# Kernel optimization log

Measured on AMD Instinct MI355X. Metric: run time of the kernel, lower is better.

The kernel has to match this reference:

```python
import jax, jax.numpy as jnp
import numpy as np

EMB = 768
HEADS = 8

def setup_inputs() -> dict:
    key = jax.random.key(0)
    ks = jax.random.split(key, 9)
    B, N, E = 16, 1024, EMB
    s = 1.0 / np.sqrt(E)
    x = jax.random.normal(ks[0], (B, N, E), dtype=jnp.float32)
    Wq = jax.random.normal(ks[1], (E, E), dtype=jnp.float32) * s
    bq = jnp.zeros((E,), dtype=jnp.float32)
    Wk = jax.random.normal(ks[2], (E, E), dtype=jnp.float32) * s
    bk = jnp.zeros((E,), dtype=jnp.float32)
    Wv = jax.random.normal(ks[3], (E, E), dtype=jnp.float32) * s
    bv = jnp.zeros((E,), dtype=jnp.float32)
    Wo = jax.random.normal(ks[4], (E, E), dtype=jnp.float32) * s
    bo = jnp.zeros((E,), dtype=jnp.float32)
    return {"x": x, "Wq": Wq, "bq": bq, "Wk": Wk, "bk": bk, "Wv": Wv, "bv": bv, "Wo": Wo, "bo": bo}

def reference(x, Wq, bq, Wk, bk, Wv, bv, Wo, bo):
    B, N, E = x.shape
    H = HEADS
    D = E // H
    # separate Q/K/V linears, split heads: b n (h d) -> b h n d
    q = (x @ Wq + bq).reshape(B, N, H, D).transpose(0, 2, 1, 3)
    k = (x @ Wk + bk).reshape(B, N, H, D).transpose(0, 2, 1, 3)
    v = (x @ Wv + bv).reshape(B, N, H, D).transpose(0, 2, 1, 3)
    energy = jnp.einsum('bhqd,bhkd->bhqk', q, k)
    # NON-STANDARD: softmax first, then divide by sqrt(emb_size)
    scaling = jnp.float32(E) ** 0.5
    attn = jax.nn.softmax(energy, axis=-1) / scaling
    out = jnp.einsum('bhqk,bhkd->bhqd', attn, v)
    out = out.transpose(0, 2, 1, 3).reshape(B, N, E)  # b h n d -> b n (h d)
    return out @ Wo + bo
```

## Files before the change

kernel.cpp:

```cpp
#include <hip/hip_runtime.h>


typedef _Float16 half8 __attribute__((ext_vector_type(8)));
typedef __fp16 fp16x2 __attribute__((ext_vector_type(2)));
typedef float f32x4 __attribute__((ext_vector_type(4)));
typedef float f32x16 __attribute__((ext_vector_type(16)));

__device__ __forceinline__ void gload_lds16(const void* g, void* l) {
  __builtin_amdgcn_global_load_lds((const __attribute__((address_space(1))) void*)g,
                                   (__attribute__((address_space(3))) void*)l, 16, 0, 0);
}


__global__ __launch_bounds__(256) void conv_x_kernel(const float* __restrict__ x,
                                                     _Float16* __restrict__ xh) {
  long i = ((long)blockIdx.x * 256 + threadIdx.x) * 8;
  float4 a = *(const float4*)(x + i);
  float4 b = *(const float4*)(x + i + 4);
  half8 o;
  o[0] = (_Float16)a.x; o[1] = (_Float16)a.y; o[2] = (_Float16)a.z; o[3] = (_Float16)a.w;
  o[4] = (_Float16)b.x; o[5] = (_Float16)b.y; o[6] = (_Float16)b.z; o[7] = (_Float16)b.w;
  *(half8*)(xh + i) = o;
}

__global__ __launch_bounds__(256) void transpose_cvt_kernel(
    const float* __restrict__ W0, const float* __restrict__ W1,
    const float* __restrict__ W2, const float* __restrict__ W3,
    _Float16* __restrict__ WT) {
  __shared__ float tile[32][33];
  int z = blockIdx.z;
  const float* W = (z == 0) ? W0 : (z == 1) ? W1 : (z == 2) ? W2 : W3;
  int k0 = blockIdx.y * 32, n0 = blockIdx.x * 32;
  int tx = threadIdx.x, ty = threadIdx.y;
#pragma unroll
  for (int j = ty; j < 32; j += 8)
    tile[j][tx] = W[(size_t)(k0 + j) * 768 + n0 + tx];
  __syncthreads();
  _Float16* dst = WT + (size_t)z * 768 * 768;
#pragma unroll
  for (int j = ty; j < 32; j += 8)
    dst[(size_t)(n0 + j) * 768 + k0 + tx] = (_Float16)tile[tx][j];
}

__global__ __launch_bounds__(256) void conv_bias_kernel(const float* __restrict__ bq,
                                                        const float* __restrict__ bk,
                                                        const float* __restrict__ bv,
                                                        float* __restrict__ bias) {
  int i = blockIdx.x * 256 + threadIdx.x;
  if (i >= 2304) return;
  bias[i] = (i < 768) ? bq[i] : (i < 1536) ? bk[i - 768] : bv[i - 1536];
}


template <int OUT_F16>
__global__ __launch_bounds__(256) void gemm_nt_kernel(
    const _Float16* __restrict__ A, const _Float16* __restrict__ Bt,
    const float* __restrict__ bias, void* __restrict__ C,
    int M, int N, int K, int ldc) {
  __shared__ _Float16 As[128 * 32];
  __shared__ _Float16 Bs[128 * 32];
  int nbx = N >> 7;
  int nwg = gridDim.x;
  int wg = blockIdx.x;
  int cpx = nwg >> 3;
  int swz = (wg & 7) * cpx + (wg >> 3);
  int bx = swz % nbx, by = swz / nbx;
  int m0 = by * 128, n0 = bx * 128;
  int t = threadIdx.x, l = t & 63, w = t >> 6;
  int lg = l >> 4, lr = l & 15;
  int wr = w >> 1, wc = w & 1;
  f32x4 acc[4][4] = {};

  for (int k0 = 0; k0 < K; k0 += 32) {
    __syncthreads();
#pragma unroll
    for (int j = 0; j < 2; ++j) {
      int slot = j * 256 + t;
      gload_lds16(A + (size_t)(m0 + (slot >> 2)) * K + k0 + (slot & 3) * 8, &As[slot * 8]);
    }
#pragma unroll
    for (int j = 0; j < 2; ++j) {
      int slot = j * 256 + t;
      gload_lds16(Bt + (size_t)(n0 + (slot >> 2)) * K + k0 + (slot & 3) * 8, &Bs[slot * 8]);
    }
    __syncthreads();
    half8 af[4], bf[4];
#pragma unroll
    for (int r = 0; r < 4; ++r) af[r] = *(const half8*)&As[(wr * 64 + r * 16 + lr) * 32 + lg * 8];
#pragma unroll
    for (int c = 0; c < 4; ++c) bf[c] = *(const half8*)&Bs[(wc * 64 + c * 16 + lr) * 32 + lg * 8];
#pragma unroll
    for (int r = 0; r < 4; ++r)
#pragma unroll
      for (int c = 0; c < 4; ++c)
        acc[r][c] = __builtin_amdgcn_mfma_f32_16x16x32_f16(af[r], bf[c], acc[r][c], 0, 0, 0);
  }

#pragma unroll
  for (int r = 0; r < 4; ++r)
#pragma unroll
    for (int c = 0; c < 4; ++c) {
      int col = n0 + wc * 64 + c * 16 + lr;
      float bb = bias[col];
#pragma unroll
      for (int i = 0; i < 4; ++i) {
        int row = m0 + wr * 64 + r * 16 + lg * 4 + i;
        float v = acc[r][c][i] + bb;
        if (OUT_F16)
          ((_Float16*)C)[(size_t)row * ldc + col] = (_Float16)v;
        else
          ((float*)C)[(size_t)row * ldc + col] = v;
      }
    }
}


__global__ __launch_bounds__(256, 3) void attn_kernel(const _Float16* __restrict__ QKV,
                                                      _Float16* __restrict__ Oh) {
  int hw = blockIdx.x;
  int lin = (hw & 7) * 128 + (hw >> 3);
  int bh = lin >> 3, qt = lin & 7;
  int b = bh >> 3, h = bh & 7;
  int t = threadIdx.x, w = t >> 6, l = t & 63;
  int lr = l & 31, hi = l >> 5;

  __shared__ __align__(16) char KF[2][12288];
  __shared__ __align__(16) _Float16 VF[2][96 * 64];

  const _Float16* Qb = QKV + (size_t)b * 1024 * 2304 + h * 96;
  const _Float16* Kb = Qb + 768;
  const _Float16* Vb = Qb + 1536;

  half8 qf[6];
  {
    int qrow = qt * 128 + w * 32 + lr;
    const _Float16 s = (_Float16)1.4426950408889634f;
#pragma unroll
    for (int c = 0; c < 6; ++c) {
      qf[c] = *(const half8*)&Qb[(size_t)qrow * 2304 + c * 16 + hi * 8];
#pragma unroll
      for (int e = 0; e < 8; ++e) qf[c][e] = qf[c][e] * s;
    }
  }

  int ks_src[3], ks_dst[3];
#pragma unroll
  for (int j = 0; j < 3; ++j) {
    int s = j * 256 + t;
    int f = s >> 6, lane = s & 63;
    int sb = f / 6, c = f - sb * 6;
    ks_src[j] = (sb * 32 + (lane & 31)) * 2304 + c * 16 + ((lane >> 5) & 1) * 8;
    ks_dst[j] = s * 16;
  }
  bool vact[2];
  int v_src[2], v_dst[2][8];
#pragma unroll
  for (int j = 0; j < 2; ++j) {
    int u = j * 256 + t;
    vact[j] = u < 384;
    int kvp = u / 12, mm = u % 12;
    v_src[j] = 2 * kvp * 2304 + mm * 8;
#pragma unroll
    for (int e = 0; e < 8; ++e) {
      int d = mm * 8 + e;
      int sw = ((d & 7) ^ ((d >> 3) & 7)) << 3;
      v_dst[j][e] = d * 64 + ((2 * kvp) ^ sw);
    }
  }

  auto stage = [&](int kv0, int bi) {
    size_t goff = (size_t)kv0 * 2304;
#pragma unroll
    for (int j = 0; j < 3; ++j)
      gload_lds16(Kb + goff + ks_src[j], &KF[bi][ks_dst[j]]);
#pragma unroll
    for (int j = 0; j < 2; ++j)
      if (vact[j]) {
        const _Float16* vp = Vb + goff + v_src[j];
        half8 v0 = *(const half8*)vp;
        half8 v1 = *(const half8*)(vp + 2304);
#pragma unroll
        for (int e = 0; e < 8; ++e) {
          union { _Float16 h2[2]; unsigned u32; } pk;
          pk.h2[0] = v0[e]; pk.h2[1] = v1[e];
          *(unsigned*)&VF[bi][v_dst[j][e]] = pk.u32;
        }
      }
  };

  float m_run = -3.0e38f, l_run = 0.f;
  f32x16 oa[3] = {};

  stage(0, 0);

  for (int tile = 0; tile < 16; ++tile) {
    int bi = tile & 1;
    __syncthreads();
    if (tile + 1 < 16) stage((tile + 1) * 64, bi ^ 1);

    f32x16 sA[2] = {};
#pragma unroll
    for (int sb = 0; sb < 2; ++sb)
#pragma unroll
      for (int c = 0; c < 6; ++c) {
        half8 kf = *(const half8*)(KF[bi] + (sb * 6 + c) * 1024 + l * 16);
        sA[sb] = __builtin_amdgcn_mfma_f32_32x32x16_f16(kf, qf[c], sA[sb], 0, 0, 0);
      }

    float tmax = -3.0e38f;
#pragma unroll
    for (int sb = 0; sb < 2; ++sb)
#pragma unroll
      for (int r = 0; r < 16; ++r) tmax = fmaxf(tmax, sA[sb][r]);
    tmax = fmaxf(tmax, __shfl_xor(tmax, 32, 64));

    if (!__all(tmax <= m_run + 11.5f)) {
      float m_new = fmaxf(m_run, tmax);
      float scale = __builtin_exp2f(m_run - m_new);
#pragma unroll
      for (int r = 0; r < 16; ++r) {
        float sr = __shfl(scale, (r & 3) + 8 * (r >> 2) + 4 * hi, 64);
        oa[0][r] *= sr; oa[1][r] *= sr; oa[2][r] *= sr;
      }
      l_run *= scale;
      m_run = m_new;
    }

    unsigned keep[8], send[8];
    float rs = 0.f;
#pragma unroll
    for (int sb = 0; sb < 2; ++sb) {
      float e[16];
#pragma unroll
      for (int r = 0; r < 16; ++r) {
        e[r] = __builtin_exp2f(sA[sb][r] - m_run);
        rs += e[r];
      }
      unsigned w32[8];
#pragma unroll
      for (int p = 0; p < 4; ++p)
#pragma unroll
        for (int m = 0; m < 2; ++m) {
          union { fp16x2 h2; unsigned u; } pk;
          pk.h2 = __builtin_amdgcn_cvt_pkrtz(e[4 * p + 2 * m], e[4 * p + 2 * m + 1]);
          w32[p * 2 + m] = pk.u;
        }
#pragma unroll
      for (int kb = 0; kb < 2; ++kb)
#pragma unroll
        for (int m = 0; m < 2; ++m) {
          keep[sb * 4 + kb * 2 + m] = hi ? w32[(2 * kb + 1) * 2 + m] : w32[(2 * kb) * 2 + m];
          send[sb * 4 + kb * 2 + m] = hi ? w32[(2 * kb) * 2 + m] : w32[(2 * kb + 1) * 2 + m];
        }
    }
    rs += __shfl_xor(rs, 32, 64);
    l_run += rs;

    unsigned recv[8];
#pragma unroll
    for (int i = 0; i < 8; ++i) recv[i] = __shfl_xor(send[i], 32, 64);

#pragma unroll
    for (int kstep = 0; kstep < 4; ++kstep) {
      int base = (kstep >> 1) * 4 + (kstep & 1) * 2;
      union { unsigned u[4]; half8 h8; } pa;
      pa.u[0] = hi ? recv[base + 0] : keep[base + 0];
      pa.u[1] = hi ? recv[base + 1] : keep[base + 1];
      pa.u[2] = hi ? keep[base + 0] : recv[base + 0];
      pa.u[3] = hi ? keep[base + 1] : recv[base + 1];
#pragma unroll
      for (int dt = 0; dt < 3; ++dt) {
        int d = dt * 32 + lr;
        int sw = ((d & 7) ^ ((d >> 3) & 7)) << 3;
        half8 vf = *(const half8*)&VF[bi][d * 64 + ((kstep * 16 + hi * 8) ^ sw)];
        oa[dt] = __builtin_amdgcn_mfma_f32_32x32x16_f16(pa.h8, vf, oa[dt], 0, 0, 0);
      }
    }
  }

  float inv = 1.0f / (l_run * 27.712812921102035f);
  size_t rbase = (size_t)(b * 1024 + qt * 128 + w * 32) * 768 + h * 96;
#pragma unroll
  for (int r = 0; r < 16; ++r) {
    int q = (r & 3) + 8 * (r >> 2) + 4 * hi;
    float ivr = __shfl(inv, q, 64);
#pragma unroll
    for (int dt = 0; dt < 3; ++dt)
      Oh[rbase + (size_t)q * 768 + dt * 32 + lr] = (_Float16)(oa[dt][r] * ivr);
  }
}


extern "C" void kernel_launch(void* const* d_in, const int* in_sizes, int n_in,
                              void* d_out, int out_size, void* d_ws, size_t ws_size,
                              hipStream_t stream) {
  const float* x  = (const float*)d_in[0];
  const float* Wq = (const float*)d_in[1];
  const float* bq = (const float*)d_in[2];
  const float* Wk = (const float*)d_in[3];
  const float* bk = (const float*)d_in[4];
  const float* Wv = (const float*)d_in[5];
  const float* bv = (const float*)d_in[6];
  const float* Wo = (const float*)d_in[7];
  const float* bo = (const float*)d_in[8];
  float* out = (float*)d_out;

  char* ws = (char*)d_ws;
  _Float16* WT   = (_Float16*)(ws);
  float*    bias = (float*)(ws + 4718592);
  _Float16* xh   = (_Float16*)(ws + 4751360);
  _Float16* QKV  = (_Float16*)(ws + 29917184);
  _Float16* Oh   = (_Float16*)(ws + 105414656);

  conv_x_kernel<<<6144, 256, 0, stream>>>(x, xh);
  transpose_cvt_kernel<<<dim3(24, 24, 4), dim3(32, 8), 0, stream>>>(Wq, Wk, Wv, Wo, WT);
  conv_bias_kernel<<<9, 256, 0, stream>>>(bq, bk, bv, bias);

  gemm_nt_kernel<1><<<2304, 256, 0, stream>>>(xh, WT, bias, QKV, 16384, 2304, 768, 2304);

  attn_kernel<<<1024, 256, 0, stream>>>(QKV, Oh);

  gemm_nt_kernel<0><<<768, 256, 0, stream>>>(Oh, WT + (size_t)2304 * 768, bo, out,
                                             16384, 768, 768, 768);
}
```

Measured before the change: 238.8 us.

## Prefetch V into registers across compute and compute softmax row sums via MFMA

The V tile for the next step is now loaded from global memory into registers before the QK and softmax compute, and written transposed into LDS only after the PV MFMAs. This hides the V global-load latency behind compute instead of stalling inside the staging step. The softmax row sum is now accumulated by an extra MFMA against a ones vector, which replaces the scalar adds and cross-lane shuffles and yields the denominator already in output layout. In exchange, register pressure rises, so the launch bound drops from 3 to 2 blocks per CU, lowering occupancy, and the row sums now come from the fp16-rounded probabilities rather than the fp32 values.

```diff
diff --git a/kernel.cpp b/kernel.cpp
--- a/kernel.cpp
+++ b/kernel.cpp
@@ -115,7 +115,7 @@
 }
 
 
-__global__ __launch_bounds__(256, 3) void attn_kernel(const _Float16* __restrict__ QKV,
+__global__ __launch_bounds__(256, 2) void attn_kernel(const _Float16* __restrict__ QKV,
                                                       _Float16* __restrict__ Oh) {
   int hw = blockIdx.x;
   int lin = (hw & 7) * 128 + (hw >> 3);
@@ -168,35 +168,57 @@
     }
   }
 
-  auto stage = [&](int kv0, int bi) {
+  auto stage_K = [&](int kv0, int bi) {
     size_t goff = (size_t)kv0 * 2304;
 #pragma unroll
     for (int j = 0; j < 3; ++j)
       gload_lds16(Kb + goff + ks_src[j], &KF[bi][ks_dst[j]]);
+  };
+
+  half8 vr0[2], vr1[2];
+  auto loadV = [&](int kv0) {
+    size_t goff = (size_t)kv0 * 2304;
 #pragma unroll
     for (int j = 0; j < 2; ++j)
       if (vact[j]) {
         const _Float16* vp = Vb + goff + v_src[j];
-        half8 v0 = *(const half8*)vp;
-        half8 v1 = *(const half8*)(vp + 2304);
+        vr0[j] = *(const half8*)vp;
+        vr1[j] = *(const half8*)(vp + 2304);
+      }
+  };
+  auto writeV = [&](int bi) {
+#pragma unroll
+    for (int j = 0; j < 2; ++j)
+      if (vact[j]) {
 #pragma unroll
         for (int e = 0; e < 8; ++e) {
           union { _Float16 h2[2]; unsigned u32; } pk;
-          pk.h2[0] = v0[e]; pk.h2[1] = v1[e];
+          pk.h2[0] = vr0[j][e]; pk.h2[1] = vr1[j][e];
           *(unsigned*)&VF[bi][v_dst[j][e]] = pk.u32;
         }
       }
   };
 
-  float m_run = -3.0e38f, l_run = 0.f;
+  half8 vones;
+#pragma unroll
+  for (int e = 0; e < 8; ++e) vones[e] = (_Float16)1.0f;
+
+  float m_run = -3.0e38f;
   f32x16 oa[3] = {};
-
-  stage(0, 0);
+  f32x16 lacc = {};
+
+  stage_K(0, 0);
+  loadV(0);
+  writeV(0);
 
   for (int tile = 0; tile < 16; ++tile) {
     int bi = tile & 1;
     __syncthreads();
-    if (tile + 1 < 16) stage((tile + 1) * 64, bi ^ 1);
+    if (tile + 1 < 16) {
+      stage_K((tile + 1) * 64, bi ^ 1);
+      loadV((tile + 1) * 64);
+      __builtin_amdgcn_sched_barrier(0);
+    }
 
     f32x16 sA[2] = {};
 #pragma unroll
@@ -221,21 +243,17 @@
       for (int r = 0; r < 16; ++r) {
         float sr = __shfl(scale, (r & 3) + 8 * (r >> 2) + 4 * hi, 64);
         oa[0][r] *= sr; oa[1][r] *= sr; oa[2][r] *= sr;
-      }
-      l_run *= scale;
+        lacc[r] *= sr;
+      }
       m_run = m_new;
     }
 
     unsigned keep[8], send[8];
-    float rs = 0.f;
 #pragma unroll
     for (int sb = 0; sb < 2; ++sb) {
       float e[16];
 #pragma unroll
-      for (int r = 0; r < 16; ++r) {
-        e[r] = __builtin_exp2f(sA[sb][r] - m_run);
-        rs += e[r];
-      }
+      for (int r = 0; r < 16; ++r) e[r] = __builtin_exp2f(sA[sb][r] - m_run);
       unsigned w32[8];
 #pragma unroll
       for (int p = 0; p < 4; ++p)
@@ -253,8 +271,6 @@
           send[sb * 4 + kb * 2 + m] = hi ? w32[(2 * kb) * 2 + m] : w32[(2 * kb + 1) * 2 + m];
         }
     }
-    rs += __shfl_xor(rs, 32, 64);
-    l_run += rs;
 
     unsigned recv[8];
 #pragma unroll
@@ -275,15 +291,17 @@
         half8 vf = *(const half8*)&VF[bi][d * 64 + ((kstep * 16 + hi * 8) ^ sw)];
         oa[dt] = __builtin_amdgcn_mfma_f32_32x32x16_f16(pa.h8, vf, oa[dt], 0, 0, 0);
       }
-    }
-  }
-
-  float inv = 1.0f / (l_run * 27.712812921102035f);
+      lacc = __builtin_amdgcn_mfma_f32_32x32x16_f16(pa.h8, vones, lacc, 0, 0, 0);
+    }
+
+    if (tile + 1 < 16) writeV(bi ^ 1);
+  }
+
   size_t rbase = (size_t)(b * 1024 + qt * 128 + w * 32) * 768 + h * 96;
 #pragma unroll
   for (int r = 0; r < 16; ++r) {
     int q = (r & 3) + 8 * (r >> 2) + 4 * hi;
-    float ivr = __shfl(inv, q, 64);
+    float ivr = 1.0f / (lacc[r] * 27.712812921102035f);
 #pragma unroll
     for (int dt = 0; dt < 3; ++dt)
       Oh[rbase + (size_t)q * 768 + dt * 32 + lr] = (_Float16)(oa[dt][r] * ivr);
```

New measurement: 232.6 us. 2.6% less time.
